# Kernel tuning notes

Hardware: AMD Instinct MI355X
Metric: run time of the kernel (lower is better)

The kernel has to match this reference:

```python
import jax, jax.numpy as jnp
import numpy as np


def _normalized_adj(A):
    # get_a: d = 0.5*I, a = off-diagonal ones + A, a2 = d @ a @ d
    off = jnp.array([[0., 1., 1.], [1., 0., 1.], [1., 1., 0.]], dtype=A.dtype)
    a = off + A
    d = 0.5 * jnp.eye(3, dtype=A.dtype)
    return d @ a @ d  # [3,3]


def setup_inputs() -> dict:
    key = jax.random.key(0)
    k1, k2 = jax.random.split(key)
    B = 8192
    x = jax.random.normal(k1, (B, 3, 10), dtype=jnp.float32)
    A = jnp.eye(3, dtype=jnp.float32)  # get_A() returns identity; Parameter init
    stdv = 1.0 / np.sqrt(10.0)
    W = jax.random.uniform(k2, (10, 10), dtype=jnp.float32, minval=-stdv, maxval=stdv)
    return {"x": x, "A": A, "W": W}


def reference(x, A, W):
    # adjacency is detached in the torch forward
    adj = jax.lax.stop_gradient(_normalized_adj(A))  # [3,3], shared across batch
    # GraphConvolution: adj @ (x @ W)
    support = jnp.einsum('bnf,fo->bno', x, W)          # [B,3,10]
    h = jnp.einsum('nm,bmo->bno', adj, support)        # [B,3,10]
    # permute -> [B,10,3]; AvgPool1d(2) on length 3 -> length 1: mean of nodes 0,1
    pooled = 0.5 * (h[:, 0, :] + h[:, 1, :])           # [B,10]
    # ScaleDotProductAttention over the batch axis
    score = jax.nn.softmax(pooled @ pooled.T, axis=-1)  # [B,B]
    v = score @ pooled                                  # [B,10]
    return v
```

## Files before the change

### kernel.cpp

```cpp
#include <hip/hip_runtime.h>
#include <math.h>

#define BROWS 8192
#define F 10
#define TJ 512
#define QP 20
#define AP 524
#define NT (BROWS / TJ)
#define IB 16
#define NW 16
#define LOG2E 1.44269504088896340736f

#if __has_builtin(__builtin_amdgcn_exp2f)
#define EXP2F(x) __builtin_amdgcn_exp2f(x)
#else
#define EXP2F(x) exp2f(x)
#endif

typedef _Float16 half4 __attribute__((ext_vector_type(4)));
typedef __fp16 fp16x2 __attribute__((ext_vector_type(2)));
typedef float floatx4 __attribute__((ext_vector_type(4)));

__device__ __forceinline__ half4 exp4_to_h4(float a, float b, float c, float d) {
#if __has_builtin(__builtin_amdgcn_cvt_pkrtz)
    union { fp16x2 h2[2]; half4 h4; } u;
    u.h2[0] = __builtin_amdgcn_cvt_pkrtz(EXP2F(a), EXP2F(b));
    u.h2[1] = __builtin_amdgcn_cvt_pkrtz(EXP2F(c), EXP2F(d));
    return u.h4;
#else
    half4 r;
    r[0] = (_Float16)EXP2F(a); r[1] = (_Float16)EXP2F(b);
    r[2] = (_Float16)EXP2F(c); r[3] = (_Float16)EXP2F(d);
    return r;
#endif
}

__device__ __forceinline__ uint32_t pack2(_Float16 a, _Float16 b) {
    union { _Float16 h[2]; uint32_t u; } x;
    x.h[0] = a; x.h[1] = b;
    return x.u;
}

__device__ __forceinline__ void gload_lds16(const void* g, void* l) {
#if __has_builtin(__builtin_amdgcn_global_load_lds)
    __builtin_amdgcn_global_load_lds(
        (const __attribute__((address_space(1))) void*)g,
        (__attribute__((address_space(3))) void*)l, 16, 0, 0);
#else
    *(float4*)l = *(const float4*)g;
#endif
}

__global__ void pooled_kernel(const float* __restrict__ x,
                              const float* __restrict__ A,
                              const float* __restrict__ W,
                              _Float16* __restrict__ poolQ,
                              _Float16* __restrict__ poolT16) {
    int b = blockIdx.x * blockDim.x + threadIdx.x;
    if (b >= BROWS) return;

    float c0 = 0.125f * (1.0f + A[0] + A[3]);
    float c1 = 0.125f * (1.0f + A[1] + A[4]);
    float c2 = 0.125f * (2.0f + A[2] + A[5]);

    const float2* xb = (const float2*)(x + (size_t)b * 3 * F);
    float xv[3 * F];
#pragma unroll
    for (int k = 0; k < 15; ++k) {
        float2 t = xb[k];
        xv[2 * k] = t.x; xv[2 * k + 1] = t.y;
    }

    float y[F];
#pragma unroll
    for (int f = 0; f < F; ++f)
        y[f] = c0 * xv[f] + c1 * xv[F + f] + c2 * xv[2 * F + f];

    float po[F];
#pragma unroll
    for (int o = 0; o < F; ++o) {
        float acc = 0.0f;
#pragma unroll
        for (int f = 0; f < F; ++f)
            acc = fmaf(y[f], W[f * F + o], acc);
        po[o] = acc;
    }

    uint2* qd = (uint2*)(poolQ + (size_t)b * QP);
    qd[0] = make_uint2(pack2((_Float16)po[0], (_Float16)po[1]),
                       pack2((_Float16)po[2], (_Float16)po[3]));
    qd[1] = make_uint2(pack2((_Float16)po[4], (_Float16)po[5]),
                       pack2((_Float16)po[6], (_Float16)po[7]));
    qd[2] = make_uint2(pack2((_Float16)po[8], (_Float16)po[9]), 0u);
    qd[3] = make_uint2(0u, 0u);
    qd[4] = make_uint2(0u, 0u);

#pragma unroll
    for (int o = 0; o < F; ++o)
        poolT16[(size_t)o * BROWS + b] = (_Float16)po[o];
    poolT16[(size_t)10 * BROWS + b] = (_Float16)1.0f;
#pragma unroll
    for (int o = 11; o < 16; ++o)
        poolT16[(size_t)o * BROWS + b] = (_Float16)0.0f;
}

__global__ void attn_kernel(const _Float16* __restrict__ poolQ,
                            const _Float16* __restrict__ poolT16,
                            float* __restrict__ out) {
    __shared__ __align__(16) _Float16 qbuf[2][TJ * QP];
    __shared__ __align__(16) _Float16 abuf[2][16 * AP];
    float* red = (float*)&qbuf[0][0];

    const int tid  = threadIdx.x;
    const int wave = tid >> 6;
    const int lane = tid & 63;
    const int m    = lane & 15;
    const int quad = lane >> 4;
    const int i0   = blockIdx.x * IB;

    half4 b1;
#pragma unroll
    for (int idx = 0; idx < 4; ++idx) {
        int f = quad * 4 + idx;
        float v = (f < F) ? (float)poolQ[(size_t)(i0 + m) * QP + f] * LOG2E : 0.0f;
        b1[idx] = (_Float16)v;
    }

    const char* qsrc0 = (const char*)poolQ + wave * 1024 + lane * 16;
    const char* qsrc1 = (const char*)poolQ + (wave + 16) * 1024 + lane * 16;
    const char* asrc  = (const char*)(poolT16 + (size_t)wave * BROWS) + lane * 16;

    char* qdst0[2] = { (char*)&qbuf[0][0] + wave * 1024 + lane * 16,
                       (char*)&qbuf[1][0] + wave * 1024 + lane * 16 };
    char* qdst1[2] = { (char*)&qbuf[0][0] + (wave + 16) * 1024 + lane * 16,
                       (char*)&qbuf[1][0] + (wave + 16) * 1024 + lane * 16 };
    char* adst[2]  = { (char*)&abuf[0][0] + wave * (AP * 2) + lane * 16,
                       (char*)&abuf[1][0] + wave * (AP * 2) + lane * 16 };

    auto dma_tile = [&](int bufi) {
        gload_lds16(qsrc0, qdst0[bufi]);
        if (wave < 4) gload_lds16(qsrc1, qdst1[bufi]);
        gload_lds16(asrc, adst[bufi]);
        qsrc0 += TJ * QP * 2;
        qsrc1 += TJ * QP * 2;
        asrc  += TJ * 2;
    };

    floatx4 acc0 = {0.f,0.f,0.f,0.f}, acc1 = {0.f,0.f,0.f,0.f};

    dma_tile(0);
    __syncthreads();

    for (int t = 0; t < NT; ++t) {
        const int buf = t & 1;
        if (t + 1 < NT) dma_tile(buf ^ 1);

#pragma unroll
        for (int c = 0; c < 2; ++c) {
            const int jb = wave * 32 + c * 16;
            half4 ag = *(const half4*)&abuf[buf][m * AP + jb + quad * 4];
            half4 a1 = *(const half4*)&qbuf[buf][(jb + m) * QP + quad * 4];
            floatx4 d1 = __builtin_amdgcn_mfma_f32_16x16x16f16(
                a1, b1, (floatx4){0.f,0.f,0.f,0.f}, 0, 0, 0);
            half4 a2 = exp4_to_h4(d1[0], d1[1], d1[2], d1[3]);
            if (c)
                acc1 = __builtin_amdgcn_mfma_f32_16x16x16f16(ag, a2, acc1, 0, 0, 0);
            else
                acc0 = __builtin_amdgcn_mfma_f32_16x16x16f16(ag, a2, acc0, 0, 0, 0);
        }
        __syncthreads();
    }

    floatx4 acc = acc0 + acc1;

    if (quad < 3)
        *(floatx4*)&red[((size_t)wave * IB + m) * 12 + quad * 4] = acc;
    __syncthreads();

    if (tid < IB * F) {
        const int i = tid / F;
        const int f = tid % F;
        float sum = 0.0f, l = 0.0f;
#pragma unroll
        for (int w = 0; w < NW; ++w) {
            sum += red[((size_t)w * IB + i) * 12 + f];
            l   += red[((size_t)w * IB + i) * 12 + 10];
        }
        out[(size_t)(i0 + i) * F + f] = sum / l;
    }
}

extern "C" void kernel_launch(void* const* d_in, const int* in_sizes, int n_in,
                              void* d_out, int out_size, void* d_ws, size_t ws_size,
                              hipStream_t stream) {
    const float* x = (const float*)d_in[0];
    const float* A = (const float*)d_in[1];
    const float* W = (const float*)d_in[2];
    float* out = (float*)d_out;

    _Float16* poolQ   = (_Float16*)d_ws;
    _Float16* poolT16 = (_Float16*)((char*)d_ws + 327680);

    pooled_kernel<<<BROWS / 64, 64, 0, stream>>>(x, A, W, poolQ, poolT16);
    attn_kernel<<<BROWS / IB, NW * 64, 0, stream>>>(poolQ, poolT16, out);
}
```

Measured before the change: 76.01 us.

## Tile pooled layout per wave and replace block barriers with per-wave vmcnt waits

Pooled features are written in a per-32-row tiled layout with a 16-half stride so each wave streams a contiguous private 2KB chunk per step into its own LDS ring slot. The per-iteration block-wide barrier is dropped in favour of waiting on the wave's own outstanding global-to-LDS loads, letting waves run independently. The log2e scale is folded as sqrt(log2e) into the stored queries, removing the separate scaled load. This relies on correct waitcnt encoding and adds fp16 rounding of pre-scaled values.

```diff
diff --git a/kernel.cpp b/kernel.cpp
--- a/kernel.cpp
+++ b/kernel.cpp
@@ -3,13 +3,10 @@
 
 #define BROWS 8192
 #define F 10
-#define TJ 512
-#define QP 20
-#define AP 524
-#define NT (BROWS / TJ)
+#define NT 16
+#define NW 16
 #define IB 16
-#define NW 16
-#define LOG2E 1.44269504088896340736f
+#define SQRT_LOG2E 1.2011224087864498f
 
 #if __has_builtin(__builtin_amdgcn_exp2f)
 #define EXP2F(x) __builtin_amdgcn_exp2f(x)
@@ -51,11 +48,23 @@
 #endif
 }
 
+__device__ __forceinline__ void wait_vm0() {
+#if __has_builtin(__builtin_amdgcn_s_waitcnt)
+    __builtin_amdgcn_s_waitcnt(0x0F70);
+#endif
+}
+
+__device__ __forceinline__ void sched_fence() {
+#if __has_builtin(__builtin_amdgcn_sched_barrier)
+    __builtin_amdgcn_sched_barrier(0);
+#endif
+}
+
 __global__ void pooled_kernel(const float* __restrict__ x,
                               const float* __restrict__ A,
                               const float* __restrict__ W,
-                              _Float16* __restrict__ poolQ,
-                              _Float16* __restrict__ poolT16) {
+                              _Float16* __restrict__ q_tiled,
+                              _Float16* __restrict__ a_tiled) {
     int b = blockIdx.x * blockDim.x + threadIdx.x;
     if (b >= BROWS) return;
 
@@ -86,30 +95,30 @@
         po[o] = acc;
     }
 
-    uint2* qd = (uint2*)(poolQ + (size_t)b * QP);
-    qd[0] = make_uint2(pack2((_Float16)po[0], (_Float16)po[1]),
-                       pack2((_Float16)po[2], (_Float16)po[3]));
-    qd[1] = make_uint2(pack2((_Float16)po[4], (_Float16)po[5]),
-                       pack2((_Float16)po[6], (_Float16)po[7]));
-    qd[2] = make_uint2(pack2((_Float16)po[8], (_Float16)po[9]), 0u);
+    float s = SQRT_LOG2E;
+    uint2* qd = (uint2*)(q_tiled + (size_t)b * 16);
+    qd[0] = make_uint2(pack2((_Float16)(s*po[0]), (_Float16)(s*po[1])),
+                       pack2((_Float16)(s*po[2]), (_Float16)(s*po[3])));
+    qd[1] = make_uint2(pack2((_Float16)(s*po[4]), (_Float16)(s*po[5])),
+                       pack2((_Float16)(s*po[6]), (_Float16)(s*po[7])));
+    qd[2] = make_uint2(pack2((_Float16)(s*po[8]), (_Float16)(s*po[9])), 0u);
     qd[3] = make_uint2(0u, 0u);
-    qd[4] = make_uint2(0u, 0u);
-
+
+    _Float16* at = a_tiled + (size_t)(b >> 5) * 512 + (b & 31);
 #pragma unroll
     for (int o = 0; o < F; ++o)
-        poolT16[(size_t)o * BROWS + b] = (_Float16)po[o];
-    poolT16[(size_t)10 * BROWS + b] = (_Float16)1.0f;
+        at[o * 32] = (_Float16)po[o];
+    at[10 * 32] = (_Float16)1.0f;
 #pragma unroll
     for (int o = 11; o < 16; ++o)
-        poolT16[(size_t)o * BROWS + b] = (_Float16)0.0f;
-}
-
-__global__ void attn_kernel(const _Float16* __restrict__ poolQ,
-                            const _Float16* __restrict__ poolT16,
+        at[o * 32] = (_Float16)0.0f;
+}
+
+__global__ void attn_kernel(const _Float16* __restrict__ q_tiled,
+                            const _Float16* __restrict__ a_tiled,
                             float* __restrict__ out) {
-    __shared__ __align__(16) _Float16 qbuf[2][TJ * QP];
-    __shared__ __align__(16) _Float16 abuf[2][16 * AP];
-    float* red = (float*)&qbuf[0][0];
+    __shared__ __align__(16) _Float16 ring[2][NW][1024];
+    float* red = (float*)&ring[0][0][0];
 
     const int tid  = threadIdx.x;
     const int wave = tid >> 6;
@@ -118,61 +127,51 @@
     const int quad = lane >> 4;
     const int i0   = blockIdx.x * IB;
 
-    half4 b1;
-#pragma unroll
-    for (int idx = 0; idx < 4; ++idx) {
-        int f = quad * 4 + idx;
-        float v = (f < F) ? (float)poolQ[(size_t)(i0 + m) * QP + f] * LOG2E : 0.0f;
-        b1[idx] = (_Float16)v;
-    }
-
-    const char* qsrc0 = (const char*)poolQ + wave * 1024 + lane * 16;
-    const char* qsrc1 = (const char*)poolQ + (wave + 16) * 1024 + lane * 16;
-    const char* asrc  = (const char*)(poolT16 + (size_t)wave * BROWS) + lane * 16;
-
-    char* qdst0[2] = { (char*)&qbuf[0][0] + wave * 1024 + lane * 16,
-                       (char*)&qbuf[1][0] + wave * 1024 + lane * 16 };
-    char* qdst1[2] = { (char*)&qbuf[0][0] + (wave + 16) * 1024 + lane * 16,
-                       (char*)&qbuf[1][0] + (wave + 16) * 1024 + lane * 16 };
-    char* adst[2]  = { (char*)&abuf[0][0] + wave * (AP * 2) + lane * 16,
-                       (char*)&abuf[1][0] + wave * (AP * 2) + lane * 16 };
-
-    auto dma_tile = [&](int bufi) {
-        gload_lds16(qsrc0, qdst0[bufi]);
-        if (wave < 4) gload_lds16(qsrc1, qdst1[bufi]);
-        gload_lds16(asrc, adst[bufi]);
-        qsrc0 += TJ * QP * 2;
-        qsrc1 += TJ * QP * 2;
-        asrc  += TJ * 2;
-    };
+    half4 b1 = *(const half4*)(q_tiled + (size_t)(i0 + m) * 16 + quad * 4);
+
+    const char* qsrc = (const char*)q_tiled + (size_t)wave * 1024 + lane * 16;
+    const char* asrc = (const char*)a_tiled + (size_t)wave * 1024 + lane * 16;
+
+    char* slot[2] = { (char*)&ring[0][wave][0] + lane * 16,
+                      (char*)&ring[1][wave][0] + lane * 16 };
 
     floatx4 acc0 = {0.f,0.f,0.f,0.f}, acc1 = {0.f,0.f,0.f,0.f};
 
-    dma_tile(0);
-    __syncthreads();
+    gload_lds16(qsrc, slot[0]);
+    gload_lds16(asrc + 0x40000  - 0x40000, slot[0] + 1024);
+    qsrc += 16 * 1024; asrc += 16 * 1024;
 
     for (int t = 0; t < NT; ++t) {
         const int buf = t & 1;
-        if (t + 1 < NT) dma_tile(buf ^ 1);
-
-#pragma unroll
-        for (int c = 0; c < 2; ++c) {
-            const int jb = wave * 32 + c * 16;
-            half4 ag = *(const half4*)&abuf[buf][m * AP + jb + quad * 4];
-            half4 a1 = *(const half4*)&qbuf[buf][(jb + m) * QP + quad * 4];
-            floatx4 d1 = __builtin_amdgcn_mfma_f32_16x16x16f16(
-                a1, b1, (floatx4){0.f,0.f,0.f,0.f}, 0, 0, 0);
-            half4 a2 = exp4_to_h4(d1[0], d1[1], d1[2], d1[3]);
-            if (c)
-                acc1 = __builtin_amdgcn_mfma_f32_16x16x16f16(ag, a2, acc1, 0, 0, 0);
-            else
-                acc0 = __builtin_amdgcn_mfma_f32_16x16x16f16(ag, a2, acc0, 0, 0, 0);
+        const _Float16* qs = &ring[buf][wave][0];
+        const _Float16* as_ = qs + 512;
+
+        wait_vm0();
+        half4 a1_0 = *(const half4*)&qs[(0 * 16 + m) * 16 + quad * 4];
+        half4 ag_0 = *(const half4*)&as_[m * 32 + 0 * 16 + quad * 4];
+        half4 a1_1 = *(const half4*)&qs[(1 * 16 + m) * 16 + quad * 4];
+        half4 ag_1 = *(const half4*)&as_[m * 32 + 1 * 16 + quad * 4];
+        sched_fence();
+
+        if (t + 1 < NT) {
+            gload_lds16(qsrc, slot[buf ^ 1]);
+            gload_lds16(asrc, slot[buf ^ 1] + 1024);
+            qsrc += 16 * 1024; asrc += 16 * 1024;
         }
-        __syncthreads();
+
+        floatx4 d1a = __builtin_amdgcn_mfma_f32_16x16x16f16(
+            a1_0, b1, (floatx4){0.f,0.f,0.f,0.f}, 0, 0, 0);
+        floatx4 d1b = __builtin_amdgcn_mfma_f32_16x16x16f16(
+            a1_1, b1, (floatx4){0.f,0.f,0.f,0.f}, 0, 0, 0);
+        half4 a2a = exp4_to_h4(d1a[0], d1a[1], d1a[2], d1a[3]);
+        half4 a2b = exp4_to_h4(d1b[0], d1b[1], d1b[2], d1b[3]);
+        acc0 = __builtin_amdgcn_mfma_f32_16x16x16f16(ag_0, a2a, acc0, 0, 0, 0);
+        acc1 = __builtin_amdgcn_mfma_f32_16x16x16f16(ag_1, a2b, acc1, 0, 0, 0);
     }
 
     floatx4 acc = acc0 + acc1;
 
+    __syncthreads();
     if (quad < 3)
         *(floatx4*)&red[((size_t)wave * IB + m) * 12 + quad * 4] = acc;
     __syncthreads();
@@ -198,9 +197,9 @@
     const float* W = (const float*)d_in[2];
     float* out = (float*)d_out;
 
-    _Float16* poolQ   = (_Float16*)d_ws;
-    _Float16* poolT16 = (_Float16*)((char*)d_ws + 327680);
-
-    pooled_kernel<<<BROWS / 64, 64, 0, stream>>>(x, A, W, poolQ, poolT16);
-    attn_kernel<<<BROWS / IB, NW * 64, 0, stream>>>(poolQ, poolT16, out);
-}
+    _Float16* q_tiled = (_Float16*)d_ws;
+    _Float16* a_tiled = (_Float16*)((char*)d_ws + 262144);
+
+    pooled_kernel<<<BROWS / 64, 64, 0, stream>>>(x, A, W, q_tiled, a_tiled);
+    attn_kernel<<<BROWS / IB, NW * 64, 0, stream>>>(q_tiled, a_tiled, out);
+}
```

Measured after the change: 82.26 us. 1.08x slower.
